# Kernel optimization log

Measured on AMD Instinct MI355X. Metric: run time of the kernel, lower is better.

Reference implementation:

```python
import jax, jax.numpy as jnp
import numpy as np


def setup_inputs() -> dict:
    key = jax.random.key(0)
    k1, k2, k3, k4, k5 = jax.random.split(key, 5)
    B, S, H, F, E = 2, 512, 1024, 3584, 8
    scale_in = 1.0 / np.sqrt(H)
    scale_ff = 1.0 / np.sqrt(F)
    return {
        "hidden_states": jax.random.normal(k1, (B, S, H), dtype=jnp.float32),
        "gate_w": jax.random.normal(k2, (E, H), dtype=jnp.float32) * scale_in,
        "w1": jax.random.normal(k3, (E, F, H), dtype=jnp.float32) * scale_in,
        "w2": jax.random.normal(k4, (E, H, F), dtype=jnp.float32) * scale_ff,
        "w3": jax.random.normal(k5, (E, F, H), dtype=jnp.float32) * scale_in,
    }


TOP_K = 2


def reference(hidden_states, gate_w, w1, w2, w3):
    B, S, H = hidden_states.shape
    E = gate_w.shape[0]
    x = hidden_states.reshape(B * S, H)  # [T, H]
    T = x.shape[0]

    # Router: softmax in fp32, top-2 selection, renormalize selected weights.
    router_logits = x @ gate_w.T  # [T, E]
    probs = jax.nn.softmax(router_logits.astype(jnp.float32), axis=-1)
    top_vals, top_idx = jax.lax.top_k(probs, TOP_K)  # [T, K]
    top_vals = top_vals / jnp.sum(top_vals, axis=-1, keepdims=True)
    top_vals = top_vals.astype(x.dtype)

    # Dense routing-weight matrix [T, E]: weight if selected else 0
    # (equivalent to the one-hot expert_mask + index_add combine).
    dense_w = jnp.zeros((T, E), dtype=x.dtype).at[
        jnp.arange(T)[:, None], top_idx
    ].add(top_vals)

    # Expert SwiGLU MLPs, batched over the expert axis.
    h1 = jnp.einsum("th,efh->etf", x, w1)  # [E, T, F]
    h3 = jnp.einsum("th,efh->etf", x, w3)  # [E, T, F]
    y = jnp.einsum("etf,ehf->eth", jax.nn.silu(h1) * h3, w2)  # [E, T, H]

    # Weighted combine across experts.
    out = jnp.einsum("eth,te->th", y, dense_w)  # [T, H]
    return out.reshape(B, S, H), router_logits
```

## Files before the change

kernel.cpp:

```cpp
#include <hip/hip_runtime.h>
#include <hip/hip_bf16.h>

typedef __bf16 v8bf __attribute__((ext_vector_type(8)));
typedef __bf16 v4bf __attribute__((ext_vector_type(4)));
typedef float  f32x4 __attribute__((ext_vector_type(4)));

#define NTOK 1024
#define HDIM 1024
#define FDIM 3584
#define NEXP 8
#define NPAIR 2048
#define MAXT1 24
#define MAXT2 40

#define OFF_COUNTS   0
#define OFF_OFFSETS  64
#define OFF_NT1      128
#define OFF_NT2      132
#define OFF_T1E      192
#define OFF_T1M      320
#define OFF_T2E      448
#define OFF_T2M      640
#define OFF_TOKIDX   1024
#define OFF_TOKWT    (1024 + 4*NPAIR)
#define OFF_PAIRTOK  (OFF_TOKWT + 4*NPAIR)
#define OFF_PAIRWT   (OFF_PAIRTOK + 4*NPAIR)
#define OFF_SLOTOF   (OFF_PAIRWT + 4*NPAIR)
#define OFF_ACT      65536
#define OFF_Y        (OFF_ACT + 2ull*NPAIR*FDIM)

static __device__ inline v4bf cvt4(float4 f) {
    v4bf r;
    r[0] = (__bf16)f.x; r[1] = (__bf16)f.y; r[2] = (__bf16)f.z; r[3] = (__bf16)f.w;
    return r;
}

#define BAR() do { asm volatile("s_waitcnt lgkmcnt(0)" ::: "memory"); \
                   __builtin_amdgcn_s_barrier(); } while (0)

__global__ __launch_bounds__(256) void moe_router(
    const float* __restrict__ x, const float* __restrict__ gw,
    float* __restrict__ logits, int* __restrict__ counts,
    int* __restrict__ tok_idx, float* __restrict__ tok_wt)
{
    const int lane = threadIdx.x & 63;
    const int wv = threadIdx.x >> 6;
    const int t = blockIdx.x * 4 + wv;
    const float* xr = x + (size_t)t * HDIM;

    float acc[NEXP];
#pragma unroll
    for (int e = 0; e < NEXP; ++e) acc[e] = 0.f;
#pragma unroll
    for (int j = 0; j < 4; ++j) {
        int h = lane * 4 + j * 256;
        float4 xv = *(const float4*)(xr + h);
#pragma unroll
        for (int e = 0; e < NEXP; ++e) {
            float4 g = *(const float4*)(gw + e * HDIM + h);
            acc[e] += xv.x * g.x + xv.y * g.y + xv.z * g.z + xv.w * g.w;
        }
    }
#pragma unroll
    for (int e = 0; e < NEXP; ++e) {
#pragma unroll
        for (int s = 32; s > 0; s >>= 1) acc[e] += __shfl_xor(acc[e], s);
    }
    if (lane == 0) {
#pragma unroll
        for (int e = 0; e < NEXP; ++e) logits[t * NEXP + e] = acc[e];
        int i0 = 0;
#pragma unroll
        for (int e = 1; e < NEXP; ++e) if (acc[e] > acc[i0]) i0 = e;
        int i1 = (i0 == 0) ? 1 : 0;
#pragma unroll
        for (int e = 0; e < NEXP; ++e) if (e != i0 && acc[e] > acc[i1]) i1 = e;
        float w0 = 1.f / (1.f + expf(acc[i1] - acc[i0]));
        float w1 = 1.f - w0;
        tok_idx[2 * t] = i0; tok_idx[2 * t + 1] = i1;
        tok_wt[2 * t] = w0;  tok_wt[2 * t + 1] = w1;
        atomicAdd(&counts[i0], 1);
        atomicAdd(&counts[i1], 1);
    }
}

__global__ void moe_scatter(const int* __restrict__ counts, const int* __restrict__ tok_idx,
                            const float* __restrict__ tok_wt, int* __restrict__ offsets,
                            int* __restrict__ pair_token, float* __restrict__ pair_wt,
                            int* __restrict__ slot_of,
                            int* __restrict__ t1e, int* __restrict__ t1m, int* __restrict__ nt1,
                            int* __restrict__ t2e, int* __restrict__ t2m, int* __restrict__ nt2)
{
    __shared__ int cur[NEXP];
    const int tid = threadIdx.x;
    if (tid == 0) {
        int run = 0, n1 = 0, n2 = 0;
        for (int e = 0; e < NEXP; ++e) {
            offsets[e] = run; cur[e] = run;
            for (int m0 = 0; m0 < counts[e]; m0 += 128) { t1e[n1] = e; t1m[n1] = m0; ++n1; }
            for (int m0 = 0; m0 < counts[e]; m0 += 64)  { t2e[n2] = e; t2m[n2] = m0; ++n2; }
            run += counts[e];
        }
        *nt1 = n1; *nt2 = n2;
    }
    __syncthreads();
    for (int p = tid; p < 2 * NTOK; p += blockDim.x) {
        int e = tok_idx[p];
        int s = atomicAdd(&cur[e], 1);
        pair_token[s] = p >> 1;
        pair_wt[s] = tok_wt[p];
        slot_of[p] = s;
    }
}

__global__ __launch_bounds__(256, 2) void moe_gemm1(
    const float* __restrict__ x, const float* __restrict__ w1g,
    const float* __restrict__ w3g, const int* __restrict__ counts,
    const int* __restrict__ offsets, const int* __restrict__ pair_token,
    const int* __restrict__ t1e, const int* __restrict__ t1m,
    const int* __restrict__ nt1,
    __bf16* __restrict__ act)
{
    const int ty = blockIdx.y;
    if (ty >= *nt1) return;
    const int e = t1e[ty];
    const int m0 = t1m[ty];
    const int Me = counts[e];
    const int rows = min(128, Me - m0);
    const int slot0 = offsets[e] + m0;
    const int n0 = blockIdx.x * 64;

    __shared__ __align__(16) __bf16 As[2][128 * 32];
    __shared__ __align__(16) __bf16 B1s[2][64 * 32];
    __shared__ __align__(16) __bf16 B3s[2][64 * 32];

    const int tid = threadIdx.x;
    const int lane = tid & 63;
    const int wv = tid >> 6;
    const int wm = (wv >> 1) * 64;
    const int wn = (wv & 1) * 32;
    const int lr = lane & 15;
    const int lk = (lane >> 4) * 8;

    f32x4 acc1[4][2], acc3[4][2];
#pragma unroll
    for (int i = 0; i < 4; ++i)
#pragma unroll
        for (int j = 0; j < 2; ++j) {
            acc1[i][j] = (f32x4){0.f, 0.f, 0.f, 0.f};
            acc3[i][j] = (f32x4){0.f, 0.f, 0.f, 0.f};
        }

    const ptrdiff_t d31 = w3g - w1g;
    const float* aptr[4];
    int awof[4];
#pragma unroll
    for (int i = 0; i < 4; ++i) {
        int slot = tid + i * 256;
        int r = slot >> 3;
        int c = (slot & 7) * 4;
        int rr = (r < rows) ? r : 0;
        aptr[i] = x + (size_t)pair_token[slot0 + rr] * HDIM + c;
        awof[i] = r * 32 + c;
    }
    const float* bp[2];
    int bwof[2];
#pragma unroll
    for (int i = 0; i < 2; ++i) {
        int slot = tid + i * 256;
        int r = slot >> 3;
        int c = (slot & 7) * 4;
        bp[i]   = w1g + ((size_t)e * FDIM + n0 + r) * HDIM + c;
        bwof[i] = r * 32 + c;
    }

    float4 a0[4], b10[2], b30[2];
    float4 a1[4], b11[2], b31[2];

#define LD1(AV, B1V, B3V, K0) do { _Pragma("unroll") \
    for (int i = 0; i < 4; ++i) AV[i] = *(const float4*)(aptr[i] + (K0)); \
    _Pragma("unroll") \
    for (int i = 0; i < 2; ++i) { B1V[i] = *(const float4*)(bp[i] + (K0)); \
                                  B3V[i] = *(const float4*)(bp[i] + d31 + (K0)); } } while (0)

#define ST1(BUF, AV, B1V, B3V) do { _Pragma("unroll") \
    for (int i = 0; i < 4; ++i) *(v4bf*)&As[BUF][awof[i]] = cvt4(AV[i]); \
    _Pragma("unroll") \
    for (int i = 0; i < 2; ++i) { *(v4bf*)&B1s[BUF][bwof[i]] = cvt4(B1V[i]); \
                                  *(v4bf*)&B3s[BUF][bwof[i]] = cvt4(B3V[i]); } } while (0)

#define CMP1(BUF) do { v8bf af[4], b1f[2], b3f[2]; _Pragma("unroll") \
    for (int i = 0; i < 4; ++i) af[i] = *(const v8bf*)&As[BUF][(wm + i * 16 + lr) * 32 + lk]; \
    _Pragma("unroll") \
    for (int i = 0; i < 2; ++i) { b1f[i] = *(const v8bf*)&B1s[BUF][(wn + i * 16 + lr) * 32 + lk]; \
                                  b3f[i] = *(const v8bf*)&B3s[BUF][(wn + i * 16 + lr) * 32 + lk]; } \
    _Pragma("unroll") \
    for (int mi = 0; mi < 4; ++mi) { _Pragma("unroll") \
        for (int ni = 0; ni < 2; ++ni) { \
            acc1[mi][ni] = __builtin_amdgcn_mfma_f32_16x16x32_bf16(af[mi], b1f[ni], acc1[mi][ni], 0, 0, 0); \
            acc3[mi][ni] = __builtin_amdgcn_mfma_f32_16x16x32_bf16(af[mi], b3f[ni], acc3[mi][ni], 0, 0, 0); } } } while (0)

    LD1(a0, b10, b30, 0);
    LD1(a1, b11, b31, 32);
    for (int k0 = 0; k0 < HDIM; k0 += 64) {
        ST1(0, a0, b10, b30);
        if (k0 + 64 < HDIM) LD1(a0, b10, b30, k0 + 64);
        BAR();
        CMP1(0);
        ST1(1, a1, b11, b31);
        if (k0 + 96 < HDIM) LD1(a1, b11, b31, k0 + 96);
        BAR();
        CMP1(1);
    }
#undef LD1
#undef ST1
#undef CMP1

    const int rj = (lane >> 4) * 4;
#pragma unroll
    for (int mi = 0; mi < 4; ++mi) {
#pragma unroll
        for (int j = 0; j < 4; ++j) {
            int rm = wm + mi * 16 + rj + j;
            if (rm < rows) {
                size_t rowoff = (size_t)(slot0 + rm) * FDIM + n0 + wn;
#pragma unroll
                for (int ni = 0; ni < 2; ++ni) {
                    float h1 = acc1[mi][ni][j];
                    float h3 = acc3[mi][ni][j];
                    float sv = (h1 / (1.f + __expf(-h1))) * h3;
                    act[rowoff + ni * 16 + lr] = (__bf16)sv;
                }
            }
        }
    }
}

__global__ __launch_bounds__(256, 4) void moe_gemm2(
    const __bf16* __restrict__ act, const float* __restrict__ w2g,
    const int* __restrict__ counts, const int* __restrict__ offsets,
    const int* __restrict__ t2e, const int* __restrict__ t2m,
    const int* __restrict__ nt2,
    float* __restrict__ y)
{
    const int ty = blockIdx.y;
    if (ty >= *nt2) return;
    const int e = t2e[ty];
    const int m0 = t2m[ty];
    const int Me = counts[e];
    const int rows = min(64, Me - m0);
    const int slot0 = offsets[e] + m0;
    const int n0 = blockIdx.x * 64;

    __shared__ __align__(16) __bf16 As[2][64 * 32];
    __shared__ __align__(16) __bf16 Bs[2][64 * 32];

    const int tid = threadIdx.x;
    const int lane = tid & 63;
    const int wv = tid >> 6;
    const int wm = (wv >> 1) * 32;
    const int wn = (wv & 1) * 32;
    const int lr = lane & 15;
    const int lk = (lane >> 4) * 8;

    f32x4 acc[2][2];
#pragma unroll
    for (int i = 0; i < 2; ++i)
#pragma unroll
        for (int j = 0; j < 2; ++j) acc[i][j] = (f32x4){0.f, 0.f, 0.f, 0.f};

    const __bf16* ap;
    int awof;
    {
        int r = tid >> 2;
        int c = (tid & 3) * 8;
        int rr = (r < rows) ? r : 0;
        ap   = act + (size_t)(slot0 + rr) * FDIM + c;
        awof = r * 32 + c;
    }
    const float* bp[2];
    int bwof[2];
#pragma unroll
    for (int i = 0; i < 2; ++i) {
        int slot = tid + i * 256;
        int r = slot >> 3;
        int c = (slot & 7) * 4;
        bp[i]   = w2g + ((size_t)e * HDIM + n0 + r) * FDIM + c;
        bwof[i] = r * 32 + c;
    }

    v8bf a8_0, a8_1;
    float4 bv0[2], bv1[2];

#define LD2(A8, BV, K0) do { A8 = *(const v8bf*)(ap + (K0)); _Pragma("unroll") \
    for (int i = 0; i < 2; ++i) BV[i] = *(const float4*)(bp[i] + (K0)); } while (0)

#define ST2(BUF, A8, BV) do { *(v8bf*)&As[BUF][awof] = A8; _Pragma("unroll") \
    for (int i = 0; i < 2; ++i) *(v4bf*)&Bs[BUF][bwof[i]] = cvt4(BV[i]); } while (0)

#define CMP2(BUF) do { v8bf af[2], bf[2]; _Pragma("unroll") \
    for (int i = 0; i < 2; ++i) { af[i] = *(const v8bf*)&As[BUF][(wm + i * 16 + lr) * 32 + lk]; \
                                  bf[i] = *(const v8bf*)&Bs[BUF][(wn + i * 16 + lr) * 32 + lk]; } \
    _Pragma("unroll") \
    for (int mi = 0; mi < 2; ++mi) { _Pragma("unroll") \
        for (int ni = 0; ni < 2; ++ni) \
            acc[mi][ni] = __builtin_amdgcn_mfma_f32_16x16x32_bf16(af[mi], bf[ni], acc[mi][ni], 0, 0, 0); } } while (0)

    LD2(a8_0, bv0, 0);
    LD2(a8_1, bv1, 32);
    for (int k0 = 0; k0 < FDIM; k0 += 64) {
        ST2(0, a8_0, bv0);
        if (k0 + 64 < FDIM) LD2(a8_0, bv0, k0 + 64);
        BAR();
        CMP2(0);
        ST2(1, a8_1, bv1);
        if (k0 + 96 < FDIM) LD2(a8_1, bv1, k0 + 96);
        BAR();
        CMP2(1);
    }
#undef LD2
#undef ST2
#undef CMP2

    const int rj = (lane >> 4) * 4;
#pragma unroll
    for (int mi = 0; mi < 2; ++mi) {
#pragma unroll
        for (int j = 0; j < 4; ++j) {
            int rm = wm + mi * 16 + rj + j;
            if (rm < rows) {
                size_t rowoff = (size_t)(slot0 + rm) * HDIM + n0 + wn;
#pragma unroll
                for (int ni = 0; ni < 2; ++ni)
                    y[rowoff + ni * 16 + lr] = acc[mi][ni][j];
            }
        }
    }
}

__global__ __launch_bounds__(256) void moe_combine(
    const float* __restrict__ y, const int* __restrict__ slot_of,
    const float* __restrict__ pair_wt, float* __restrict__ out)
{
    const int t = blockIdx.x;
    const int tid = threadIdx.x;
    const int s0 = slot_of[2 * t];
    const int s1 = slot_of[2 * t + 1];
    const float w0 = pair_wt[s0];
    const float w1 = pair_wt[s1];
    const float4 a = *(const float4*)(y + (size_t)s0 * HDIM + tid * 4);
    const float4 b = *(const float4*)(y + (size_t)s1 * HDIM + tid * 4);
    float4 o;
    o.x = w0 * a.x + w1 * b.x;
    o.y = w0 * a.y + w1 * b.y;
    o.z = w0 * a.z + w1 * b.z;
    o.w = w0 * a.w + w1 * b.w;
    *(float4*)(out + (size_t)t * HDIM + tid * 4) = o;
}

extern "C" void kernel_launch(void* const* d_in, const int* in_sizes, int n_in,
                              void* d_out, int out_size, void* d_ws, size_t ws_size,
                              hipStream_t stream) {
    const float* x   = (const float*)d_in[0];
    const float* gw  = (const float*)d_in[1];
    const float* w1  = (const float*)d_in[2];
    const float* w2  = (const float*)d_in[3];
    const float* w3  = (const float*)d_in[4];

    float* out    = (float*)d_out;
    float* logits = out + (size_t)NTOK * HDIM;

    char* ws = (char*)d_ws;
    int*    counts     = (int*)(ws + OFF_COUNTS);
    int*    offsets    = (int*)(ws + OFF_OFFSETS);
    int*    nt1        = (int*)(ws + OFF_NT1);
    int*    nt2        = (int*)(ws + OFF_NT2);
    int*    t1e        = (int*)(ws + OFF_T1E);
    int*    t1m        = (int*)(ws + OFF_T1M);
    int*    t2e        = (int*)(ws + OFF_T2E);
    int*    t2m        = (int*)(ws + OFF_T2M);
    int*    tok_idx    = (int*)(ws + OFF_TOKIDX);
    float*  tok_wt     = (float*)(ws + OFF_TOKWT);
    int*    pair_token = (int*)(ws + OFF_PAIRTOK);
    float*  pair_wt    = (float*)(ws + OFF_PAIRWT);
    int*    slot_of    = (int*)(ws + OFF_SLOTOF);
    __bf16* act        = (__bf16*)(ws + OFF_ACT);
    float*  yb         = (float*)(ws + OFF_Y);

    hipMemsetAsync(counts, 0, 64, stream);

    moe_router<<<dim3(NTOK / 4), dim3(256), 0, stream>>>(x, gw, logits, counts, tok_idx, tok_wt);
    moe_scatter<<<dim3(1), dim3(256), 0, stream>>>(counts, tok_idx, tok_wt, offsets,
                                                   pair_token, pair_wt, slot_of,
                                                   t1e, t1m, nt1, t2e, t2m, nt2);
    moe_gemm1<<<dim3(FDIM / 64, MAXT1), dim3(256), 0, stream>>>(
        x, w1, w3, counts, offsets, pair_token, t1e, t1m, nt1, act);
    moe_gemm2<<<dim3(HDIM / 64, MAXT2), dim3(256), 0, stream>>>(
        act, w2, counts, offsets, t2e, t2m, nt2, yb);
    moe_combine<<<dim3(NTOK), dim3(256), 0, stream>>>(yb, slot_of, pair_wt, out);
}
```

Baseline: 210.4 us.

## Pre-convert tokens to bf16, pad LDS rows, raise GEMM occupancy bounds

Adds a kernel that converts the fp32 hidden states to bf16 once, so gemm1 loads bf16 token rows directly instead of reloading and converting fp32 rows for every F tile. LDS tiles in both GEMMs get a padded row stride of 40 elements to reduce bank conflicts on the MFMA fragment reads. Launch bounds rise to 3 and 6 blocks per CU to push more occupancy. The changes add an extra kernel launch and a workspace buffer, and the padding uses more LDS, which could limit the occupancy the new bounds ask for.

```diff
diff --git a/kernel.cpp b/kernel.cpp
--- a/kernel.cpp
+++ b/kernel.cpp
@@ -12,6 +12,7 @@
 #define NPAIR 2048
 #define MAXT1 24
 #define MAXT2 40
+#define LDP 40
 
 #define OFF_COUNTS   0
 #define OFF_OFFSETS  64
@@ -26,7 +27,8 @@
 #define OFF_PAIRTOK  (OFF_TOKWT + 4*NPAIR)
 #define OFF_PAIRWT   (OFF_PAIRTOK + 4*NPAIR)
 #define OFF_SLOTOF   (OFF_PAIRWT + 4*NPAIR)
-#define OFF_ACT      65536
+#define OFF_XB       65536
+#define OFF_ACT      (OFF_XB + 2ull*NTOK*HDIM)
 #define OFF_Y        (OFF_ACT + 2ull*NPAIR*FDIM)
 
 static __device__ inline v4bf cvt4(float4 f) {
@@ -37,6 +39,14 @@
 
 #define BAR() do { asm volatile("s_waitcnt lgkmcnt(0)" ::: "memory"); \
                    __builtin_amdgcn_s_barrier(); } while (0)
+
+__global__ __launch_bounds__(256) void moe_cvtx(const float* __restrict__ x,
+                                                __bf16* __restrict__ xb)
+{
+    const size_t i = ((size_t)blockIdx.x * 256 + threadIdx.x) * 4;
+    float4 v = *(const float4*)(x + i);
+    *(v4bf*)(xb + i) = cvt4(v);
+}
 
 __global__ __launch_bounds__(256) void moe_router(
     const float* __restrict__ x, const float* __restrict__ gw,
@@ -113,8 +123,8 @@
     }
 }
 
-__global__ __launch_bounds__(256, 2) void moe_gemm1(
-    const float* __restrict__ x, const float* __restrict__ w1g,
+__global__ __launch_bounds__(256, 3) void moe_gemm1(
+    const __bf16* __restrict__ xb, const float* __restrict__ w1g,
     const float* __restrict__ w3g, const int* __restrict__ counts,
     const int* __restrict__ offsets, const int* __restrict__ pair_token,
     const int* __restrict__ t1e, const int* __restrict__ t1m,
@@ -130,9 +140,9 @@
     const int slot0 = offsets[e] + m0;
     const int n0 = blockIdx.x * 64;
 
-    __shared__ __align__(16) __bf16 As[2][128 * 32];
-    __shared__ __align__(16) __bf16 B1s[2][64 * 32];
-    __shared__ __align__(16) __bf16 B3s[2][64 * 32];
+    __shared__ __align__(16) __bf16 As[2][128 * LDP];
+    __shared__ __align__(16) __bf16 B1s[2][64 * LDP];
+    __shared__ __align__(16) __bf16 B3s[2][64 * LDP];
 
     const int tid = threadIdx.x;
     const int lane = tid & 63;
@@ -152,16 +162,16 @@
         }
 
     const ptrdiff_t d31 = w3g - w1g;
-    const float* aptr[4];
-    int awof[4];
-#pragma unroll
-    for (int i = 0; i < 4; ++i) {
+    const __bf16* aptr[2];
+    int awof[2];
+#pragma unroll
+    for (int i = 0; i < 2; ++i) {
         int slot = tid + i * 256;
-        int r = slot >> 3;
-        int c = (slot & 7) * 4;
+        int r = slot >> 2;
+        int c = (slot & 3) * 8;
         int rr = (r < rows) ? r : 0;
-        aptr[i] = x + (size_t)pair_token[slot0 + rr] * HDIM + c;
-        awof[i] = r * 32 + c;
+        aptr[i] = xb + (size_t)pair_token[slot0 + rr] * HDIM + c;
+        awof[i] = r * LDP + c;
     }
     const float* bp[2];
     int bwof[2];
@@ -171,29 +181,27 @@
         int r = slot >> 3;
         int c = (slot & 7) * 4;
         bp[i]   = w1g + ((size_t)e * FDIM + n0 + r) * HDIM + c;
-        bwof[i] = r * 32 + c;
-    }
-
-    float4 a0[4], b10[2], b30[2];
-    float4 a1[4], b11[2], b31[2];
+        bwof[i] = r * LDP + c;
+    }
+
+    v8bf a0[2], a1[2];
+    float4 b10[2], b30[2], b11[2], b31[2];
 
 #define LD1(AV, B1V, B3V, K0) do { _Pragma("unroll") \
-    for (int i = 0; i < 4; ++i) AV[i] = *(const float4*)(aptr[i] + (K0)); \
+    for (int i = 0; i < 2; ++i) { AV[i] = *(const v8bf*)(aptr[i] + (K0)); \
+                                  B1V[i] = *(const float4*)(bp[i] + (K0)); \
+                                  B3V[i] = *(const float4*)(bp[i] + d31 + (K0)); } } while (0)
+
+#define ST1(BUF, AV, B1V, B3V) do { _Pragma("unroll") \
+    for (int i = 0; i < 2; ++i) { *(v8bf*)&As[BUF][awof[i]] = AV[i]; \
+                                  *(v4bf*)&B1s[BUF][bwof[i]] = cvt4(B1V[i]); \
+                                  *(v4bf*)&B3s[BUF][bwof[i]] = cvt4(B3V[i]); } } while (0)
+
+#define CMP1(BUF) do { v8bf af[4], b1f[2], b3f[2]; _Pragma("unroll") \
+    for (int i = 0; i < 4; ++i) af[i] = *(const v8bf*)&As[BUF][(wm + i * 16 + lr) * LDP + lk]; \
     _Pragma("unroll") \
-    for (int i = 0; i < 2; ++i) { B1V[i] = *(const float4*)(bp[i] + (K0)); \
-                                  B3V[i] = *(const float4*)(bp[i] + d31 + (K0)); } } while (0)
-
-#define ST1(BUF, AV, B1V, B3V) do { _Pragma("unroll") \
-    for (int i = 0; i < 4; ++i) *(v4bf*)&As[BUF][awof[i]] = cvt4(AV[i]); \
-    _Pragma("unroll") \
-    for (int i = 0; i < 2; ++i) { *(v4bf*)&B1s[BUF][bwof[i]] = cvt4(B1V[i]); \
-                                  *(v4bf*)&B3s[BUF][bwof[i]] = cvt4(B3V[i]); } } while (0)
-
-#define CMP1(BUF) do { v8bf af[4], b1f[2], b3f[2]; _Pragma("unroll") \
-    for (int i = 0; i < 4; ++i) af[i] = *(const v8bf*)&As[BUF][(wm + i * 16 + lr) * 32 + lk]; \
-    _Pragma("unroll") \
-    for (int i = 0; i < 2; ++i) { b1f[i] = *(const v8bf*)&B1s[BUF][(wn + i * 16 + lr) * 32 + lk]; \
-                                  b3f[i] = *(const v8bf*)&B3s[BUF][(wn + i * 16 + lr) * 32 + lk]; } \
+    for (int i = 0; i < 2; ++i) { b1f[i] = *(const v8bf*)&B1s[BUF][(wn + i * 16 + lr) * LDP + lk]; \
+                                  b3f[i] = *(const v8bf*)&B3s[BUF][(wn + i * 16 + lr) * LDP + lk]; } \
     _Pragma("unroll") \
     for (int mi = 0; mi < 4; ++mi) { _Pragma("unroll") \
         for (int ni = 0; ni < 2; ++ni) { \
@@ -236,7 +244,7 @@
     }
 }
 
-__global__ __launch_bounds__(256, 4) void moe_gemm2(
+__global__ __launch_bounds__(256, 6) void moe_gemm2(
     const __bf16* __restrict__ act, const float* __restrict__ w2g,
     const int* __restrict__ counts, const int* __restrict__ offsets,
     const int* __restrict__ t2e, const int* __restrict__ t2m,
@@ -252,8 +260,8 @@
     const int slot0 = offsets[e] + m0;
     const int n0 = blockIdx.x * 64;
 
-    __shared__ __align__(16) __bf16 As[2][64 * 32];
-    __shared__ __align__(16) __bf16 Bs[2][64 * 32];
+    __shared__ __align__(16) __bf16 As[2][64 * LDP];
+    __shared__ __align__(16) __bf16 Bs[2][64 * LDP];
 
     const int tid = threadIdx.x;
     const int lane = tid & 63;
@@ -276,7 +284,7 @@
         int c = (tid & 3) * 8;
         int rr = (r < rows) ? r : 0;
         ap   = act + (size_t)(slot0 + rr) * FDIM + c;
-        awof = r * 32 + c;
+        awof = r * LDP + c;
     }
     const float* bp[2];
     int bwof[2];
@@ -286,7 +294,7 @@
         int r = slot >> 3;
         int c = (slot & 7) * 4;
         bp[i]   = w2g + ((size_t)e * HDIM + n0 + r) * FDIM + c;
-        bwof[i] = r * 32 + c;
+        bwof[i] = r * LDP + c;
     }
 
     v8bf a8_0, a8_1;
@@ -299,8 +307,8 @@
     for (int i = 0; i < 2; ++i) *(v4bf*)&Bs[BUF][bwof[i]] = cvt4(BV[i]); } while (0)
 
 #define CMP2(BUF) do { v8bf af[2], bf[2]; _Pragma("unroll") \
-    for (int i = 0; i < 2; ++i) { af[i] = *(const v8bf*)&As[BUF][(wm + i * 16 + lr) * 32 + lk]; \
-                                  bf[i] = *(const v8bf*)&Bs[BUF][(wn + i * 16 + lr) * 32 + lk]; } \
+    for (int i = 0; i < 2; ++i) { af[i] = *(const v8bf*)&As[BUF][(wm + i * 16 + lr) * LDP + lk]; \
+                                  bf[i] = *(const v8bf*)&Bs[BUF][(wn + i * 16 + lr) * LDP + lk]; } \
     _Pragma("unroll") \
     for (int mi = 0; mi < 2; ++mi) { _Pragma("unroll") \
         for (int ni = 0; ni < 2; ++ni) \
@@ -384,17 +392,19 @@
     int*    pair_token = (int*)(ws + OFF_PAIRTOK);
     float*  pair_wt    = (float*)(ws + OFF_PAIRWT);
     int*    slot_of    = (int*)(ws + OFF_SLOTOF);
+    __bf16* xb         = (__bf16*)(ws + OFF_XB);
     __bf16* act        = (__bf16*)(ws + OFF_ACT);
     float*  yb         = (float*)(ws + OFF_Y);
 
     hipMemsetAsync(counts, 0, 64, stream);
 
+    moe_cvtx<<<dim3(NTOK * HDIM / 1024), dim3(256), 0, stream>>>(x, xb);
     moe_router<<<dim3(NTOK / 4), dim3(256), 0, stream>>>(x, gw, logits, counts, tok_idx, tok_wt);
     moe_scatter<<<dim3(1), dim3(256), 0, stream>>>(counts, tok_idx, tok_wt, offsets,
                                                    pair_token, pair_wt, slot_of,
                                                    t1e, t1m, nt1, t2e, t2m, nt2);
     moe_gemm1<<<dim3(FDIM / 64, MAXT1), dim3(256), 0, stream>>>(
-        x, w1, w3, counts, offsets, pair_token, t1e, t1m, nt1, act);
+        xb, w1, w3, counts, offsets, pair_token, t1e, t1m, nt1, act);
     moe_gemm2<<<dim3(HDIM / 64, MAXT2), dim3(256), 0, stream>>>(
         act, w2, counts, offsets, t2e, t2m, nt2, yb);
     moe_combine<<<dim3(NTOK), dim3(256), 0, stream>>>(yb, slot_of, pair_wt, out);
```

After: 285.6 us. 35.8% more time.
